# Kernel tuning notes

Hardware: AMD Instinct MI355X
Metric: run time of the kernel (lower is better)

## Reference

```python
import jax, jax.numpy as jnp
import numpy as np

WS = (7, 7, 7)          # window size (S, H, W)
NUM_HEADS = 6
DIM = 192
B_, NW = 128, 32        # total windows, windows per image (mask dim)
N = WS[0] * WS[1] * WS[2]  # 343 tokens per window


def _relative_position_index():
    # Faithful replica of the torch __init__ logic (incl. indexing='xy' and
    # the 3*W1-1 / 2*W1-1 multipliers).
    cs = np.arange(WS[0]); ch = np.arange(WS[1]); cw = np.arange(WS[2])
    coords = np.stack(np.meshgrid(cs, ch, cw, indexing='xy'))  # (3, Wh, Ws, Ww)
    cf = coords.reshape(3, -1)                                  # (3, N)
    rel = cf[:, :, None] - cf[:, None, :]                       # (3, N, N)
    rel = rel.transpose(1, 2, 0).astype(np.int64)               # (N, N, 3)
    rel[:, :, 0] += WS[0] - 1
    rel[:, :, 1] += WS[1] - 1
    rel[:, :, 2] += WS[2] - 1
    rel[:, :, 0] *= 3 * WS[1] - 1
    rel[:, :, 1] *= 2 * WS[1] - 1
    return rel.sum(-1)                                          # (N, N) int


def setup_inputs() -> dict:
    key = jax.random.key(0)
    ks = jax.random.split(key, 6)
    C = DIM
    x = jax.random.normal(ks[0], (B_, N, C), dtype=jnp.float32)
    mask = jax.random.normal(ks[1], (NW, N, N), dtype=jnp.float32)
    qkv_w = jax.random.normal(ks[2], (3 * C, C), dtype=jnp.float32) * 0.02
    qkv_b = jnp.zeros((3 * C,), dtype=jnp.float32)
    proj_w = jax.random.normal(ks[3], (C, C), dtype=jnp.float32) * 0.02
    proj_b = jnp.zeros((C,), dtype=jnp.float32)
    table_len = (2 * WS[0] - 1) * (2 * WS[1] - 1) * (2 * WS[2] - 1)
    rpb_table = jax.random.normal(ks[4], (table_len, NUM_HEADS), dtype=jnp.float32) * 0.02
    rel_index = jnp.asarray(_relative_position_index(), dtype=jnp.int32)
    return {"x": x, "mask": mask, "qkv_w": qkv_w, "qkv_b": qkv_b,
            "proj_w": proj_w, "proj_b": proj_b, "rpb_table": rpb_table,
            "rel_index": rel_index}


def reference(x, mask, qkv_w, qkv_b, proj_w, proj_b, rpb_table, rel_index):
    B, n, C = x.shape
    H = NUM_HEADS
    hd = C // H
    scale = hd ** (-0.5)
    qkv = x @ qkv_w.T + qkv_b                      # (B, N, 3C)
    qkv = qkv.reshape(B, n, 3, H, hd).transpose(2, 0, 3, 1, 4)  # (3, B, H, N, hd)
    q, k, v = qkv[0] * scale, qkv[1], qkv[2]
    attn = jnp.einsum('bhnd,bhmd->bhnm', q, k)     # (B, H, N, N)
    bias = rpb_table[rel_index.reshape(-1)].reshape(n, n, H)
    attn = attn + bias.transpose(2, 0, 1)[None]    # (B, H, N, N)
    nW = mask.shape[0]
    attn = attn.reshape(B // nW, nW, H, n, n) + mask[None, :, None]
    attn = jax.nn.softmax(attn.reshape(B, H, n, n), axis=-1)
    out = jnp.einsum('bhnm,bhmd->bhnd', attn, v)   # (B, H, N, hd)
    out = out.transpose(0, 2, 1, 3).reshape(B, n, C)
    return out @ proj_w.T + proj_b
```

## Files before the change

kernel.cpp:

```cpp
#include <hip/hip_runtime.h>
#include <hip/hip_fp16.h>
#include <hip/hip_bf16.h>
#include <stdint.h>

#define WN 343
#define NH 6
#define HD 32
#define CD 192
#define NB 128
#define NWM 32
#define BMROW 352
#define BMSLICE (11*16*BMROW)
#define BMKC (16*BMROW)
#define LOG2E 1.4426950408889634f

typedef __attribute__((ext_vector_type(8))) short short8;
typedef __attribute__((ext_vector_type(4))) float f32x4;

__device__ __forceinline__ unsigned short f2bf(float f) {
  union { float f; uint32_t u; } v; v.f = f;
  uint32_t r = v.u + 0x7fffu + ((v.u >> 16) & 1u);
  return (unsigned short)(r >> 16);
}

__device__ __forceinline__ uint32_t pk2bf(float a, float b) {
  __hip_bfloat162 h = __float22bfloat162_rn(make_float2(a, b));
  return *(uint32_t*)&h;
}

__device__ __forceinline__ uint32_t pkh2(float a, float b) {
  __half2 h; h.x = __float2half(a); h.y = __float2half(b);
  return *(uint32_t*)&h;
}

typedef const __attribute__((address_space(1))) unsigned int* gas_ptr;
typedef __attribute__((address_space(3))) unsigned int* las_ptr;
__device__ __forceinline__ void gload16(const unsigned short* g, unsigned short* l) {
  __builtin_amdgcn_global_load_lds((gas_ptr)(const void*)g, (las_ptr)(void*)l, 16, 0, 0);
}

__global__ __launch_bounds__(256) void prep_kernel(
    const float* __restrict__ wq, const float* __restrict__ wp,
    unsigned short* __restrict__ wqb, unsigned short* __restrict__ wpb,
    const int* __restrict__ rel, const float* __restrict__ rpb,
    const float* __restrict__ mask, uint32_t* __restrict__ bP,
    uint32_t* __restrict__ mP, const float* __restrict__ x,
    unsigned short* __restrict__ xb) {
  __shared__ float M[352][33];
  const int bid = blockIdx.x;
  const int tid = threadIdx.x;
  if (bid < 66 + 352) {
    const bool isBias = (bid < 66);
    const int sub = isBias ? bid : bid - 66;
    const int grp = sub / 11;
    const int kc = sub - grp * 11;
    const int k0 = kc * 32;
    const float* mw = mask + (size_t)grp * (WN * WN);
    for (int idx = tid; idx < 352 * 32; idx += 256) {
      int n = idx >> 5, k = idx & 31;
      float v;
      if (isBias) {
        int nc = (n < WN) ? n : (WN - 1);
        v = (k0 + k < WN) ? rpb[rel[nc * WN + k0 + k] * NH + grp] * LOG2E
                          : -30000.0f;
      } else {
        v = (n < WN && k0 + k < WN) ? mw[n * WN + k0 + k] * LOG2E : 0.0f;
      }
      M[n][k] = v;
    }
    __syncthreads();
    uint32_t* outp = (isBias ? bP : mP) + (size_t)grp * BMSLICE + (size_t)kc * BMKC;
#pragma unroll
    for (int quad = 0; quad < 4; ++quad) {
#pragma unroll
      for (int j = 0; j < 2; ++j) {
        int n = tid + 256 * j;
        if (n < 352) {
          uint4 o;
          o.x = pkh2(M[n][quad * 8 + 0], M[n][quad * 8 + 4]);
          o.y = pkh2(M[n][quad * 8 + 1], M[n][quad * 8 + 5]);
          o.z = pkh2(M[n][quad * 8 + 2], M[n][quad * 8 + 6]);
          o.w = pkh2(M[n][quad * 8 + 3], M[n][quad * 8 + 7]);
          *(uint4*)(outp + ((size_t)quad * 352 + n) * 4) = o;
        }
      }
    }
    return;
  }
  int cb = bid - 418;
  if (cb < 54) {
    int g = cb * 256 + tid;
    int sk = g / 768; int rem = g - sk * 768;
    int row = rem >> 2; int cc = rem & 3;
    int s = sk / 6; int kt = sk - s * 6;
    int lch = cc ^ ((row >> 1) & 3);
    const float* src = wq + (size_t)(s * 192 + row) * CD + kt * 32 + lch * 8;
    f32x4 a = *(const f32x4*)src;
    f32x4 b = *(const f32x4*)(src + 4);
    union { short8 v8; uint32_t d[4]; } pk;
    pk.d[0] = pk2bf(a[0], a[1]);
    pk.d[1] = pk2bf(a[2], a[3]);
    pk.d[2] = pk2bf(b[0], b[1]);
    pk.d[3] = pk2bf(b[2], b[3]);
    *(short8*)(wqb + (size_t)g * 8) = pk.v8;
    return;
  }
  cb -= 54;
  if (cb < 36) {
    int i4 = (cb * 256 + tid) * 4;
    f32x4 v = *(const f32x4*)(wp + i4);
    union { uint2 u2; uint32_t d[2]; } o;
    o.d[0] = pk2bf(v[0], v[1]);
    o.d[1] = pk2bf(v[2], v[3]);
    *(uint2*)(wpb + i4) = o.u2;
    return;
  }
  cb -= 36;
  size_t gx = (size_t)cb * 256 + tid;
  int tile = (int)(gx >> 9); int rem = (int)(gx & 511);
  int row = rem >> 2; int cc = rem & 3;
  int mb = tile / 6; int kt = tile - mb * 6;
  int lch = cc ^ ((row >> 1) & 3);
  const float* src = x + ((size_t)mb * 128 + row) * CD + kt * 32 + lch * 8;
  f32x4 a = *(const f32x4*)src;
  f32x4 b = *(const f32x4*)(src + 4);
  union { short8 v8; uint32_t d[4]; } pk;
  pk.d[0] = pk2bf(a[0], a[1]);
  pk.d[1] = pk2bf(a[2], a[3]);
  pk.d[2] = pk2bf(b[0], b[1]);
  pk.d[3] = pk2bf(b[2], b[3]);
  *(short8*)(xb + gx * 8) = pk.v8;
}

__global__ __launch_bounds__(256) void qkv_kernel(
    const unsigned short* __restrict__ xb, const unsigned short* __restrict__ wqb,
    const float* __restrict__ bvec,
    unsigned short* __restrict__ qb, unsigned short* __restrict__ kb,
    unsigned short* __restrict__ vb) {
  __shared__ __align__(16) unsigned short SL[10240];
  unsigned short* XL = SL;
  unsigned short* WL = SL + 4096;
  const int tid = threadIdx.x;
  const int wave = tid >> 6, lane = tid & 63;
  const int quad = lane >> 4, c = lane & 15;
  const int m0 = blockIdx.x * 128;
  const int s = blockIdx.y;
  const int chk = (quad ^ ((c >> 1) & 3)) * 8;

  f32x4 acc[2][12];
#pragma unroll
  for (int i = 0; i < 2; ++i)
#pragma unroll
    for (int j = 0; j < 12; ++j) acc[i][j] = (f32x4){0.f, 0.f, 0.f, 0.f};

  const size_t xt0 = (size_t)blockIdx.x * 6;
  const size_t wt0 = (size_t)s * 6;
  for (int kt = 0; kt < 6; ++kt) {
    const unsigned short* gx = xb + ((xt0 + kt) << 12) + tid * 8;
    const unsigned short* gw = wqb + (wt0 + kt) * 6144 + tid * 8;
    unsigned short* lx = XL + (size_t)wave * 512;
    unsigned short* lw = WL + (size_t)wave * 512;
    gload16(gx, lx);
    gload16(gx + 2048, lx + 2048);
    gload16(gw, lw);
    gload16(gw + 2048, lw + 2048);
    gload16(gw + 4096, lw + 4096);
    __syncthreads();
    short8 af0 = *(const short8*)&XL[(wave * 32 + c) * 32 + chk];
    short8 af1 = *(const short8*)&XL[(wave * 32 + 16 + c) * 32 + chk];
#pragma unroll
    for (int j = 0; j < 12; ++j) {
      short8 bfr = *(const short8*)&WL[(j * 16 + c) * 32 + chk];
      acc[0][j] = __builtin_amdgcn_mfma_f32_16x16x32_bf16(af0, bfr, acc[0][j], 0, 0, 0);
      acc[1][j] = __builtin_amdgcn_mfma_f32_16x16x32_bf16(af1, bfr, acc[1][j], 0, 0, 0);
    }
    __syncthreads();
  }

  const float qscale = 0.25503486f;
  unsigned short* dst = (s == 0) ? qb : ((s == 1) ? kb : vb);
  const float scl = (s == 0) ? qscale : 1.0f;
  const int n0 = s * 192;
  unsigned short* Lh0 = SL;
  unsigned short* Lh1 = SL + 4608;
  for (int hh = 0; hh < 3; ++hh) {
    __syncthreads();
#pragma unroll
    for (int jj = 0; jj < 4; ++jj) {
      int j = hh * 4 + jj;
      int hl = jj >> 1;
      int dd = (jj & 1) * 16 + c;
      float bn = bvec[n0 + j * 16 + c];
      unsigned short* L = hl ? Lh1 : Lh0;
#pragma unroll
      for (int i = 0; i < 2; ++i)
#pragma unroll
        for (int r = 0; r < 4; ++r) {
          int m = wave * 32 + i * 16 + quad * 4 + r;
          L[m * 36 + dd] = f2bf((acc[i][j][r] + bn) * scl);
        }
    }
    __syncthreads();
    const int m = tid & 127;
    const int hl = tid >> 7;
    const int M = m0 + m;
    const int b = M / WN;
    const int tok = M - b * WN;
    const int h = hh * 2 + hl;
    const unsigned short* L = hl ? Lh1 : Lh0;
    unsigned short* drow = dst + (((size_t)b * NH + h) * WN + tok) * HD;
#pragma unroll
    for (int t2 = 0; t2 < 4; ++t2) {
      int d0 = t2 * 8;
      *(short8*)&drow[d0] = *(const short8*)&L[m * 36 + d0];
    }
  }
}

__global__ __launch_bounds__(512) void attn_kernel(
    const unsigned short* __restrict__ qb, const unsigned short* __restrict__ kb,
    const unsigned short* __restrict__ vb, const uint32_t* __restrict__ biasP,
    const uint32_t* __restrict__ maskP, unsigned short* __restrict__ ob) {
  __shared__ __align__(16) unsigned short Ks[352][40];
  __shared__ __align__(16) unsigned short Vt[HD][360];
  const int bid = blockIdx.x;
  const int job = (bid & 7) * 96 + (bid >> 3);
  const int wdx = job / 24;
  const int inner = job - wdx * 24;
  const int h = inner >> 2;
  const int b = (inner & 3) * 32 + wdx;
  const int tid = threadIdx.x;
  const int wave = tid >> 6, lane = tid & 63;
  const int quad = lane >> 4, c = lane & 15;
  const size_t base = ((size_t)b * NH + h) * (WN * HD);
  const unsigned short* q = qb + base;
  const unsigned short* k = kb + base;
  const unsigned short* v = vb + base;
  const uint32_t* bP = biasP + (size_t)h * BMSLICE;
  const uint32_t* mP = maskP + (size_t)wdx * BMSLICE;

  for (int t = tid; t < WN * 4; t += 512) {
    int r = t >> 2, ch = t & 3;
    int kk = r & 31;
    int row = (r & ~31) + 16 * ((kk >> 2) & 1) + 4 * (kk >> 3) + (kk & 3);
    *(short8*)&Ks[row][ch * 8] = *(const short8*)(k + r * HD + ch * 8);
  }
  for (int t = tid; t < 9 * 32; t += 512) {
    int kg = WN + (t >> 5);
    int kk = kg & 31;
    int row = (kg & ~31) + 16 * ((kk >> 2) & 1) + 4 * (kk >> 3) + (kk & 3);
    Ks[row][t & 31] = 0;
  }
  for (int t = tid; t < WN; t += 512) {
#pragma unroll
    for (int ch = 0; ch < 4; ++ch) {
      short8 vv = *(const short8*)(v + t * HD + ch * 8);
#pragma unroll
      for (int j = 0; j < 8; ++j) Vt[ch * 8 + j][t] = vv[j];
    }
  }
  for (int t = tid; t < 9 * 32; t += 512) {
    Vt[t & 31][WN + (t >> 5)] = 0;
  }
  __syncthreads();

  for (int qt = wave; qt < 22; qt += 8) {
    const int q0 = qt * 16;
    int qr = q0 + c; if (qr > WN - 1) qr = WN - 1;
    const short8 qf = *(const short8*)(q + qr * HD + quad * 8);
    const uint32_t* bRow = bP + ((size_t)quad * 352 + q0 + c) * 4;
    const uint32_t* mRow = mP + ((size_t)quad * 352 + q0 + c) * 4;

    f32x4 o0 = (f32x4){0.f, 0.f, 0.f, 0.f}, o1 = (f32x4){0.f, 0.f, 0.f, 0.f};
    float l = 0.f;
#pragma unroll
    for (int kc = 0; kc < 11; ++kc) {
      uint4 bw4 = *(const uint4*)(bRow + (size_t)kc * BMKC);
      uint4 mw4 = *(const uint4*)(mRow + (size_t)kc * BMKC);
      f32x4 cc0, cc1;
      {
        __half2 s2; float2 f;
        s2 = __hadd2(*(__half2*)&bw4.x, *(__half2*)&mw4.x);
        f = __half22float2(s2); cc0[0] = f.x; cc1[0] = f.y;
        s2 = __hadd2(*(__half2*)&bw4.y, *(__half2*)&mw4.y);
        f = __half22float2(s2); cc0[1] = f.x; cc1[1] = f.y;
        s2 = __hadd2(*(__half2*)&bw4.z, *(__half2*)&mw4.z);
        f = __half22float2(s2); cc0[2] = f.x; cc1[2] = f.y;
        s2 = __hadd2(*(__half2*)&bw4.w, *(__half2*)&mw4.w);
        f = __half22float2(s2); cc0[3] = f.x; cc1[3] = f.y;
      }
      const int k0 = kc * 32;
      short8 kf0 = *(const short8*)&Ks[k0 + c][quad * 8];
      short8 kf1 = *(const short8*)&Ks[k0 + 16 + c][quad * 8];
      f32x4 s0 = __builtin_amdgcn_mfma_f32_16x16x32_bf16(kf0, qf, cc0, 0, 0, 0);
      f32x4 s1 = __builtin_amdgcn_mfma_f32_16x16x32_bf16(kf1, qf, cc1, 0, 0, 0);
      float p0 = __builtin_amdgcn_exp2f(s0[0]), p1 = __builtin_amdgcn_exp2f(s0[1]);
      float p2 = __builtin_amdgcn_exp2f(s0[2]), p3 = __builtin_amdgcn_exp2f(s0[3]);
      float p4 = __builtin_amdgcn_exp2f(s1[0]), p5 = __builtin_amdgcn_exp2f(s1[1]);
      float p6 = __builtin_amdgcn_exp2f(s1[2]), p7 = __builtin_amdgcn_exp2f(s1[3]);
      l += (p0 + p1 + p2 + p3) + (p4 + p5 + p6 + p7);
      union { short8 v8; uint32_t d[4]; } pf;
      pf.d[0] = pk2bf(p0, p1);
      pf.d[1] = pk2bf(p2, p3);
      pf.d[2] = pk2bf(p4, p5);
      pf.d[3] = pk2bf(p6, p7);
      short8 vf0 = *(const short8*)&Vt[c][k0 + quad * 8];
      short8 vf1 = *(const short8*)&Vt[16 + c][k0 + quad * 8];
      o0 = __builtin_amdgcn_mfma_f32_16x16x32_bf16(pf.v8, vf0, o0, 0, 0, 0);
      o1 = __builtin_amdgcn_mfma_f32_16x16x32_bf16(pf.v8, vf1, o1, 0, 0, 0);
    }
    l += __shfl_xor(l, 16);
    l += __shfl_xor(l, 32);

#pragma unroll
    for (int r = 0; r < 4; ++r) {
      int n = q0 + quad * 4 + r;
      if (n < WN) {
        float lq = __shfl(l, quad * 4 + r, 16);
        float inv = 1.0f / lq;
        size_t orow = ((size_t)b * WN + n) * CD + h * HD;
        ob[orow + c] = f2bf(o0[r] * inv);
        ob[orow + 16 + c] = f2bf(o1[r] * inv);
      }
    }
  }
}

__global__ __launch_bounds__(256) void proj_kernel(
    const unsigned short* __restrict__ ob, const unsigned short* __restrict__ wpb,
    const float* __restrict__ bvec, float* __restrict__ out) {
  __shared__ __align__(16) unsigned short Xs[64][40];
  __shared__ __align__(16) unsigned short Ws[192][40];
  const int tid = threadIdx.x;
  const int wave = tid >> 6, lane = tid & 63;
  const int quad = lane >> 4, c = lane & 15;
  const int m0 = blockIdx.x * 64;

  f32x4 acc[12];
#pragma unroll
  for (int j = 0; j < 12; ++j) acc[j] = (f32x4){0.f, 0.f, 0.f, 0.f};

  for (int kt = 0; kt < 6; ++kt) {
    const int k0 = kt * 32;
    {
      int r = tid >> 2, ch = tid & 3;
      *(short8*)&Xs[r][ch * 8] =
          *(const short8*)(ob + (size_t)(m0 + r) * CD + k0 + ch * 8);
    }
#pragma unroll
    for (int it = 0; it < 3; ++it) {
      int r = it * 64 + (tid >> 2), ch = tid & 3;
      *(short8*)&Ws[r][ch * 8] =
          *(const short8*)(wpb + (size_t)r * CD + k0 + ch * 8);
    }
    __syncthreads();
    short8 af = *(const short8*)&Xs[wave * 16 + c][quad * 8];
#pragma unroll
    for (int j = 0; j < 12; ++j) {
      short8 bfr = *(const short8*)&Ws[j * 16 + c][quad * 8];
      acc[j] = __builtin_amdgcn_mfma_f32_16x16x32_bf16(af, bfr, acc[j], 0, 0, 0);
    }
    __syncthreads();
  }

#pragma unroll
  for (int j = 0; j < 12; ++j) {
    int col = j * 16 + c;
    float bn = bvec[col];
#pragma unroll
    for (int r = 0; r < 4; ++r) {
      int m = m0 + wave * 16 + quad * 4 + r;
      out[(size_t)m * CD + col] = acc[j][r] + bn;
    }
  }
}

extern "C" void kernel_launch(void* const* d_in, const int* in_sizes, int n_in,
                              void* d_out, int out_size, void* d_ws, size_t ws_size,
                              hipStream_t stream) {
  const float* x      = (const float*)d_in[0];
  const float* mask   = (const float*)d_in[1];
  const float* qkv_w  = (const float*)d_in[2];
  const float* qkv_b  = (const float*)d_in[3];
  const float* proj_w = (const float*)d_in[4];
  const float* proj_b = (const float*)d_in[5];
  const float* rpb    = (const float*)d_in[6];
  const int*   rel    = (const int*)d_in[7];
  float* out = (float*)d_out;

  char* ws = (char*)d_ws;
  uint32_t* biasP = (uint32_t*)ws;
  size_t off = 1486848;
  uint32_t* maskP = (uint32_t*)(ws + off); off += 7929856;
  unsigned short* qb = (unsigned short*)(ws + off); off += 16859136;
  unsigned short* kb = (unsigned short*)(ws + off); off += 16859136;
  unsigned short* vb = (unsigned short*)(ws + off); off += 16859136;
  unsigned short* obuf = (unsigned short*)(ws + off); off += 16859136;
  unsigned short* wqb = (unsigned short*)(ws + off); off += 221184;
  unsigned short* wpb = (unsigned short*)(ws + off); off += 73728;
  unsigned short* xb  = (unsigned short*)(ws + off); off += 16859136;

  hipLaunchKernelGGL(prep_kernel, dim3(418 + 54 + 36 + 4116), dim3(256), 0, stream,
                     qkv_w, proj_w, wqb, wpb, rel, rpb, mask, biasP, maskP, x, xb);
  hipLaunchKernelGGL(qkv_kernel, dim3(343, 3), dim3(256), 0, stream,
                     xb, wqb, qkv_b, qb, kb, vb);
  hipLaunchKernelGGL(attn_kernel, dim3(NH * NB), dim3(512), 0, stream,
                     qb, kb, vb, biasP, maskP, obuf);
  hipLaunchKernelGGL(proj_kernel, dim3(686), dim3(256), 0, stream,
                     obuf, wpb, proj_b, out);
}
```

Before: 220.0 us.

## Pre-combine bias and mask per window-head; swizzled tiled layout for proj input

The prep kernel now writes one fp16 table per (window, head) holding rel-pos bias plus mask, so the attention inner loop loads a single packed word set and skips the half2 add. The attention output and proj weights are stored in a swizzled 128x32 tile layout, which lets the proj kernel fill LDS with direct global-to-LDS 16-byte loads instead of going through registers. The cost is a larger combined table (32x6 slices instead of 6+32) that is written once and read from memory, plus a scattered store pattern in the attention epilogue.

```diff
diff --git a/kernel.cpp b/kernel.cpp
--- a/kernel.cpp
+++ b/kernel.cpp
@@ -43,51 +43,67 @@
     const float* __restrict__ wq, const float* __restrict__ wp,
     unsigned short* __restrict__ wqb, unsigned short* __restrict__ wpb,
     const int* __restrict__ rel, const float* __restrict__ rpb,
-    const float* __restrict__ mask, uint32_t* __restrict__ bP,
-    uint32_t* __restrict__ mP, const float* __restrict__ x,
-    unsigned short* __restrict__ xb) {
-  __shared__ float M[352][33];
+    const float* __restrict__ mask, uint32_t* __restrict__ bmP,
+    const float* __restrict__ x, unsigned short* __restrict__ xb) {
   const int bid = blockIdx.x;
   const int tid = threadIdx.x;
-  if (bid < 66 + 352) {
-    const bool isBias = (bid < 66);
-    const int sub = isBias ? bid : bid - 66;
-    const int grp = sub / 11;
-    const int kc = sub - grp * 11;
+  if (bid < 352) {
+    __shared__ __half M16[352][33];
+    __shared__ unsigned short R[WN][33];
+    const int wdx = bid / 11;
+    const int kc = bid - wdx * 11;
     const int k0 = kc * 32;
-    const float* mw = mask + (size_t)grp * (WN * WN);
+    const float* mw = mask + (size_t)wdx * (WN * WN);
     for (int idx = tid; idx < 352 * 32; idx += 256) {
       int n = idx >> 5, k = idx & 31;
-      float v;
-      if (isBias) {
-        int nc = (n < WN) ? n : (WN - 1);
-        v = (k0 + k < WN) ? rpb[rel[nc * WN + k0 + k] * NH + grp] * LOG2E
-                          : -30000.0f;
-      } else {
-        v = (n < WN && k0 + k < WN) ? mw[n * WN + k0 + k] * LOG2E : 0.0f;
-      }
-      M[n][k] = v;
-    }
-    __syncthreads();
-    uint32_t* outp = (isBias ? bP : mP) + (size_t)grp * BMSLICE + (size_t)kc * BMKC;
+      float v = (n < WN && k0 + k < WN) ? mw[n * WN + k0 + k] : 0.0f;
+      M16[n][k] = __float2half(v);
+    }
+    for (int idx = tid; idx < WN * 32; idx += 256) {
+      int n = idx >> 5, k = idx & 31;
+      R[n][k] = (unsigned short)((k0 + k < WN) ? rel[n * WN + k0 + k] : 0);
+    }
+    __syncthreads();
+    uint32_t* outB = bmP + (size_t)(wdx * 6) * BMSLICE + (size_t)kc * BMKC;
 #pragma unroll
     for (int quad = 0; quad < 4; ++quad) {
+      const int q8 = quad * 8;
 #pragma unroll
       for (int j = 0; j < 2; ++j) {
         int n = tid + 256 * j;
         if (n < 352) {
-          uint4 o;
-          o.x = pkh2(M[n][quad * 8 + 0], M[n][quad * 8 + 4]);
-          o.y = pkh2(M[n][quad * 8 + 1], M[n][quad * 8 + 5]);
-          o.z = pkh2(M[n][quad * 8 + 2], M[n][quad * 8 + 6]);
-          o.w = pkh2(M[n][quad * 8 + 3], M[n][quad * 8 + 7]);
-          *(uint4*)(outp + ((size_t)quad * 352 + n) * 4) = o;
+          int nc = (n < WN) ? n : (WN - 1);
+          float vA[4], vB[4]; int rA[4], rB[4]; bool oA[4], oB[4];
+#pragma unroll
+          for (int r = 0; r < 4; ++r) {
+            vA[r] = __half2float(M16[n][q8 + r]);
+            vB[r] = __half2float(M16[n][q8 + r + 4]);
+            rA[r] = (int)R[nc][q8 + r] * NH;
+            rB[r] = (int)R[nc][q8 + r + 4] * NH;
+            oA[r] = (k0 + q8 + r) < WN;
+            oB[r] = (k0 + q8 + r + 4) < WN;
+          }
+#pragma unroll
+          for (int h = 0; h < 6; ++h) {
+            float a[4], b[4];
+#pragma unroll
+            for (int r = 0; r < 4; ++r) {
+              a[r] = oA[r] ? (vA[r] + rpb[rA[r] + h]) * LOG2E : -30000.0f;
+              b[r] = oB[r] ? (vB[r] + rpb[rB[r] + h]) * LOG2E : -30000.0f;
+            }
+            uint4 o;
+            o.x = pkh2(a[0], b[0]);
+            o.y = pkh2(a[1], b[1]);
+            o.z = pkh2(a[2], b[2]);
+            o.w = pkh2(a[3], b[3]);
+            *(uint4*)(outB + (size_t)h * BMSLICE + ((size_t)quad * 352 + n) * 4) = o;
+          }
         }
       }
     }
     return;
   }
-  int cb = bid - 418;
+  int cb = bid - 352;
   if (cb < 54) {
     int g = cb * 256 + tid;
     int sk = g / 768; int rem = g - sk * 768;
@@ -106,16 +122,23 @@
     return;
   }
   cb -= 54;
-  if (cb < 36) {
-    int i4 = (cb * 256 + tid) * 4;
-    f32x4 v = *(const f32x4*)(wp + i4);
-    union { uint2 u2; uint32_t d[2]; } o;
-    o.d[0] = pk2bf(v[0], v[1]);
-    o.d[1] = pk2bf(v[2], v[3]);
-    *(uint2*)(wpb + i4) = o.u2;
+  if (cb < 18) {
+    int g = cb * 256 + tid;
+    int kt = g / 768; int rem = g - kt * 768;
+    int row = rem >> 2; int cc = rem & 3;
+    int lch = cc ^ ((row >> 1) & 3);
+    const float* src = wp + (size_t)row * CD + kt * 32 + lch * 8;
+    f32x4 a = *(const f32x4*)src;
+    f32x4 b = *(const f32x4*)(src + 4);
+    union { short8 v8; uint32_t d[4]; } pk;
+    pk.d[0] = pk2bf(a[0], a[1]);
+    pk.d[1] = pk2bf(a[2], a[3]);
+    pk.d[2] = pk2bf(b[0], b[1]);
+    pk.d[3] = pk2bf(b[2], b[3]);
+    *(short8*)(wpb + (size_t)g * 8) = pk.v8;
     return;
   }
-  cb -= 36;
+  cb -= 18;
   size_t gx = (size_t)cb * 256 + tid;
   int tile = (int)(gx >> 9); int rem = (int)(gx & 511);
   int row = rem >> 2; int cc = rem & 3;
@@ -219,8 +242,8 @@
 
 __global__ __launch_bounds__(512) void attn_kernel(
     const unsigned short* __restrict__ qb, const unsigned short* __restrict__ kb,
-    const unsigned short* __restrict__ vb, const uint32_t* __restrict__ biasP,
-    const uint32_t* __restrict__ maskP, unsigned short* __restrict__ ob) {
+    const unsigned short* __restrict__ vb, const uint32_t* __restrict__ bmP,
+    unsigned short* __restrict__ ob) {
   __shared__ __align__(16) unsigned short Ks[352][40];
   __shared__ __align__(16) unsigned short Vt[HD][360];
   const int bid = blockIdx.x;
@@ -236,8 +259,7 @@
   const unsigned short* q = qb + base;
   const unsigned short* k = kb + base;
   const unsigned short* v = vb + base;
-  const uint32_t* bP = biasP + (size_t)h * BMSLICE;
-  const uint32_t* mP = maskP + (size_t)wdx * BMSLICE;
+  const uint32_t* bmS = bmP + (size_t)(wdx * 6 + h) * BMSLICE;
 
   for (int t = tid; t < WN * 4; t += 512) {
     int r = t >> 2, ch = t & 3;
@@ -268,26 +290,20 @@
     const int q0 = qt * 16;
     int qr = q0 + c; if (qr > WN - 1) qr = WN - 1;
     const short8 qf = *(const short8*)(q + qr * HD + quad * 8);
-    const uint32_t* bRow = bP + ((size_t)quad * 352 + q0 + c) * 4;
-    const uint32_t* mRow = mP + ((size_t)quad * 352 + q0 + c) * 4;
+    const uint32_t* bmRow = bmS + ((size_t)quad * 352 + q0 + c) * 4;
 
     f32x4 o0 = (f32x4){0.f, 0.f, 0.f, 0.f}, o1 = (f32x4){0.f, 0.f, 0.f, 0.f};
     float l = 0.f;
 #pragma unroll
     for (int kc = 0; kc < 11; ++kc) {
-      uint4 bw4 = *(const uint4*)(bRow + (size_t)kc * BMKC);
-      uint4 mw4 = *(const uint4*)(mRow + (size_t)kc * BMKC);
+      uint4 w4 = *(const uint4*)(bmRow + (size_t)kc * BMKC);
       f32x4 cc0, cc1;
       {
-        __half2 s2; float2 f;
-        s2 = __hadd2(*(__half2*)&bw4.x, *(__half2*)&mw4.x);
-        f = __half22float2(s2); cc0[0] = f.x; cc1[0] = f.y;
-        s2 = __hadd2(*(__half2*)&bw4.y, *(__half2*)&mw4.y);
-        f = __half22float2(s2); cc0[1] = f.x; cc1[1] = f.y;
-        s2 = __hadd2(*(__half2*)&bw4.z, *(__half2*)&mw4.z);
-        f = __half22float2(s2); cc0[2] = f.x; cc1[2] = f.y;
-        s2 = __hadd2(*(__half2*)&bw4.w, *(__half2*)&mw4.w);
-        f = __half22float2(s2); cc0[3] = f.x; cc1[3] = f.y;
+        float2 f;
+        f = __half22float2(*(__half2*)&w4.x); cc0[0] = f.x; cc1[0] = f.y;
+        f = __half22float2(*(__half2*)&w4.y); cc0[1] = f.x; cc1[1] = f.y;
+        f = __half22float2(*(__half2*)&w4.z); cc0[2] = f.x; cc1[2] = f.y;
+        f = __half22float2(*(__half2*)&w4.w); cc0[3] = f.x; cc1[3] = f.y;
       }
       const int k0 = kc * 32;
       short8 kf0 = *(const short8*)&Ks[k0 + c][quad * 8];
@@ -318,46 +334,50 @@
       if (n < WN) {
         float lq = __shfl(l, quad * 4 + r, 16);
         float inv = 1.0f / lq;
-        size_t orow = ((size_t)b * WN + n) * CD + h * HD;
-        ob[orow + c] = f2bf(o0[r] * inv);
-        ob[orow + 16 + c] = f2bf(o1[r] * inv);
+        int M = b * WN + n;
+        int rloc = M & 127;
+        int xr = (rloc >> 1) & 3;
+        size_t base2 = (((size_t)(M >> 7) * 6 + h) << 12) + rloc * 32;
+        ob[base2 + (((c >> 3) ^ xr) << 3) + (c & 7)] = f2bf(o0[r] * inv);
+        ob[base2 + ((((c >> 3) | 2) ^ xr) << 3) + (c & 7)] = f2bf(o1[r] * inv);
       }
     }
   }
 }
 
 __global__ __launch_bounds__(256) void proj_kernel(
-    const unsigned short* __restrict__ ob, const unsigned short* __restrict__ wpb,
+    const unsigned short* __restrict__ obp, const unsigned short* __restrict__ wpb,
     const float* __restrict__ bvec, float* __restrict__ out) {
-  __shared__ __align__(16) unsigned short Xs[64][40];
-  __shared__ __align__(16) unsigned short Ws[192][40];
+  __shared__ __align__(16) unsigned short SL[8192];
+  unsigned short* XL = SL;
+  unsigned short* WL = SL + 2048;
   const int tid = threadIdx.x;
   const int wave = tid >> 6, lane = tid & 63;
   const int quad = lane >> 4, c = lane & 15;
   const int m0 = blockIdx.x * 64;
+  const int mb = blockIdx.x >> 1;
+  const int r0 = (blockIdx.x & 1) * 64;
+  const int chk = (quad ^ ((c >> 1) & 3)) * 8;
 
   f32x4 acc[12];
 #pragma unroll
   for (int j = 0; j < 12; ++j) acc[j] = (f32x4){0.f, 0.f, 0.f, 0.f};
 
   for (int kt = 0; kt < 6; ++kt) {
-    const int k0 = kt * 32;
-    {
-      int r = tid >> 2, ch = tid & 3;
-      *(short8*)&Xs[r][ch * 8] =
-          *(const short8*)(ob + (size_t)(m0 + r) * CD + k0 + ch * 8);
-    }
-#pragma unroll
-    for (int it = 0; it < 3; ++it) {
-      int r = it * 64 + (tid >> 2), ch = tid & 3;
-      *(short8*)&Ws[r][ch * 8] =
-          *(const short8*)(wpb + (size_t)r * CD + k0 + ch * 8);
-    }
-    __syncthreads();
-    short8 af = *(const short8*)&Xs[wave * 16 + c][quad * 8];
+    const unsigned short* gx =
+        obp + (((size_t)mb * 6 + kt) << 12) + r0 * 32 + tid * 8;
+    const unsigned short* gw = wpb + (size_t)kt * 6144 + tid * 8;
+    unsigned short* lx = XL + (size_t)wave * 512;
+    unsigned short* lw = WL + (size_t)wave * 512;
+    gload16(gx, lx);
+    gload16(gw, lw);
+    gload16(gw + 2048, lw + 2048);
+    gload16(gw + 4096, lw + 4096);
+    __syncthreads();
+    short8 af = *(const short8*)&XL[(wave * 16 + c) * 32 + chk];
 #pragma unroll
     for (int j = 0; j < 12; ++j) {
-      short8 bfr = *(const short8*)&Ws[j * 16 + c][quad * 8];
+      short8 bfr = *(const short8*)&WL[(j * 16 + c) * 32 + chk];
       acc[j] = __builtin_amdgcn_mfma_f32_16x16x32_bf16(af, bfr, acc[j], 0, 0, 0);
     }
     __syncthreads();
@@ -389,9 +409,8 @@
   float* out = (float*)d_out;
 
   char* ws = (char*)d_ws;
-  uint32_t* biasP = (uint32_t*)ws;
-  size_t off = 1486848;
-  uint32_t* maskP = (uint32_t*)(ws + off); off += 7929856;
+  uint32_t* bmP = (uint32_t*)ws;
+  size_t off = 47579136;
   unsigned short* qb = (unsigned short*)(ws + off); off += 16859136;
   unsigned short* kb = (unsigned short*)(ws + off); off += 16859136;
   unsigned short* vb = (unsigned short*)(ws + off); off += 16859136;
@@ -400,12 +419,12 @@
   unsigned short* wpb = (unsigned short*)(ws + off); off += 73728;
   unsigned short* xb  = (unsigned short*)(ws + off); off += 16859136;
 
-  hipLaunchKernelGGL(prep_kernel, dim3(418 + 54 + 36 + 4116), dim3(256), 0, stream,
-                     qkv_w, proj_w, wqb, wpb, rel, rpb, mask, biasP, maskP, x, xb);
+  hipLaunchKernelGGL(prep_kernel, dim3(352 + 54 + 18 + 4116), dim3(256), 0, stream,
+                     qkv_w, proj_w, wqb, wpb, rel, rpb, mask, bmP, x, xb);
   hipLaunchKernelGGL(qkv_kernel, dim3(343, 3), dim3(256), 0, stream,
                      xb, wqb, qkv_b, qb, kb, vb);
   hipLaunchKernelGGL(attn_kernel, dim3(NH * NB), dim3(512), 0, stream,
-                     qb, kb, vb, biasP, maskP, obuf);
+                     qb, kb, vb, bmP, obuf);
   hipLaunchKernelGGL(proj_kernel, dim3(686), dim3(256), 0, stream,
                      obuf, wpb, proj_b, out);
 }
```

Result: slower. 260.9 us (+18.6%).
